# Kernel tuning notes

Measured on AMD Instinct MI355X. Metric: run time of the kernel, lower is better.

The kernel has to match this reference:

```python
import math
import jax, jax.numpy as jnp
import numpy as np

D_EMBD = 1024
N_HEAD = 16
BLOCK = 2048
B, T = 4, 2048


def setup_inputs() -> dict:
    key = jax.random.key(0)
    ks = jax.random.split(key, 5)
    d = D_EMBD
    return {
        "x": jax.random.normal(ks[0], (B, T, d), dtype=jnp.float32),
        "Wq": jax.random.normal(ks[1], (d, d), dtype=jnp.float32),
        "bq": jnp.zeros((d,), dtype=jnp.float32),
        "Wk": jax.random.normal(ks[2], (d, d), dtype=jnp.float32),
        "bk": jnp.zeros((d,), dtype=jnp.float32),
        "Wv": jax.random.normal(ks[3], (d, d), dtype=jnp.float32),
        "bv": jnp.zeros((d,), dtype=jnp.float32),
        "Wp": jax.random.normal(ks[4], (d, d), dtype=jnp.float32),
        "bp": jnp.zeros((d,), dtype=jnp.float32),
    }


def reference(x, Wq, bq, Wk, bk, Wv, bv, Wp, bp):
    Bb, Tt, C = x.shape
    n_head = N_HEAD
    hd = C // n_head  # head dim
    # QKV projections -> [B, H, T, hd]
    def split_heads(y):
        return y.reshape(Bb, Tt, n_head, hd).transpose(0, 2, 1, 3)
    Q = split_heads(x @ Wq + bq)
    K = split_heads(x @ Wk + bk)
    V = split_heads(x @ Wv + bv)
    # scores [B, H, T, T]
    attn = jnp.einsum('bhqd,bhkd->bhqk', Q, K) / math.sqrt(hd)
    # causal mask: -inf strictly above diagonal (matches triu(ones*-inf, 1))
    causal = jnp.tril(jnp.ones((Tt, Tt), dtype=bool))
    attn = jnp.where(causal, attn, -jnp.inf)
    attn = jax.nn.softmax(attn, axis=-1)
    y = jnp.einsum('bhqk,bhkd->bhqd', attn, V)
    y = y.transpose(0, 2, 1, 3).reshape(Bb, Tt, C)
    return y @ Wp + bp
```

## Files before the change

kernel.cpp:

```cpp
#include <hip/hip_runtime.h>
#include <stdint.h>
#include <stddef.h>

#define TT 2048
#define CC 1024
#define BBATCH 4
#define HH 16
#define HD 64
#define MTOT (BBATCH * TT)

typedef __bf16 bf16_t;
typedef __bf16 bf16x4 __attribute__((ext_vector_type(4)));
typedef __bf16 bf16x8 __attribute__((ext_vector_type(8)));
typedef float f32x4 __attribute__((ext_vector_type(4)));
typedef float f32x16 __attribute__((ext_vector_type(16)));

typedef const __attribute__((address_space(1))) uint32_t* as1_u32p;
typedef __attribute__((address_space(3))) uint32_t* as3_u32p;

__device__ __forceinline__ f32x4 mfma16(bf16x8 a, bf16x8 b, f32x4 c) {
  return __builtin_amdgcn_mfma_f32_16x16x32_bf16(a, b, c, 0, 0, 0);
}
__device__ __forceinline__ f32x16 mfma32(bf16x8 a, bf16x8 b, f32x16 c) {
  return __builtin_amdgcn_mfma_f32_32x32x16_bf16(a, b, c, 0, 0, 0);
}

__device__ __forceinline__ void gload_lds16(void* lds, const void* g) {
  __builtin_amdgcn_global_load_lds((as1_u32p)g, (as3_u32p)lds, 16, 0, 0);
}

__device__ __forceinline__ bf16x8 rd32(const char* t, int row, int lane) {
  int sl = (lane >> 4) ^ ((row >> 1) & 3);
  return *(const bf16x8*)(t + row * 64 + sl * 16);
}
__device__ __forceinline__ bf16x8 rd32r(const char* t, int row, int slot) {
  return *(const bf16x8*)(t + row * 128 + ((slot ^ (row & 7)) * 16));
}

__global__ void split_x_kernel(const float* __restrict__ x, bf16_t* __restrict__ xh,
                               bf16_t* __restrict__ xl, int n4) {
  int stride = gridDim.x * blockDim.x;
  for (int i = blockIdx.x * blockDim.x + threadIdx.x; i < n4; i += stride) {
    float4 v = ((const float4*)x)[i];
    float vv[4] = {v.x, v.y, v.z, v.w};
    bf16x4 hv, lv;
#pragma unroll
    for (int j = 0; j < 4; ++j) {
      bf16_t h = (bf16_t)vv[j];
      hv[j] = h;
      lv[j] = (bf16_t)(vv[j] - (float)h);
    }
    *(bf16x4*)(xh + (size_t)i * 4) = hv;
    *(bf16x4*)(xl + (size_t)i * 4) = lv;
  }
}

__global__ void transpose_split_kernel(const float* __restrict__ Wq, const float* __restrict__ Wk,
                                       const float* __restrict__ Wv, const float* __restrict__ Wp,
                                       bf16_t* __restrict__ wqkh, bf16_t* __restrict__ wqkl,
                                       bf16_t* __restrict__ wv_t, bf16_t* __restrict__ wp_t) {
  __shared__ float tile[32][33];
  int mat = blockIdx.z;
  const float* W = (mat == 0) ? Wq : (mat == 1) ? Wk : (mat == 2) ? Wv : Wp;
  int tx = threadIdx.x, ty = threadIdx.y;
  int n0 = blockIdx.x * 32, k0 = blockIdx.y * 32;
#pragma unroll
  for (int j = 0; j < 32; j += 8)
    tile[ty + j][tx] = W[(size_t)(k0 + ty + j) * CC + n0 + tx];
  __syncthreads();
#pragma unroll
  for (int j = 0; j < 32; j += 8) {
    float v = tile[tx][ty + j];
    int n = n0 + ty + j, k = k0 + tx;
    if (mat <= 1) {
      bf16_t h = (bf16_t)v;
      size_t o = (size_t)(mat * CC + n) * CC + k;
      wqkh[o] = h;
      wqkl[o] = (bf16_t)(v - (float)h);
    } else {
      bf16_t* dst = (mat == 2) ? wv_t : wp_t;
      dst[(size_t)n * CC + k] = (bf16_t)v;
    }
  }
}

__global__ __launch_bounds__(512, 2) void gemm_qk_kernel(
    const bf16_t* __restrict__ Ah, const bf16_t* __restrict__ Al,
    const bf16_t* __restrict__ Bh, const bf16_t* __restrict__ Bl,
    const float* __restrict__ bq, const float* __restrict__ bk,
    bf16_t* __restrict__ qh, bf16_t* __restrict__ ql,
    bf16_t* __restrict__ kh, bf16_t* __restrict__ kl) {
  __shared__ __align__(16) char s_ah[2][16384];
  __shared__ __align__(16) char s_al[2][16384];
  __shared__ __align__(16) char s_bh[2][16384];
  __shared__ __align__(16) char s_bl[2][16384];

  const int blk = blockIdx.x;
  const int bn = blk & 7;
  const int bm = blk >> 3;
  const int tid = threadIdx.x, w = tid >> 6, lane = tid & 63;
  const int wr = w >> 2, wc = w & 3;
  const int qi = lane & 15, hi = lane >> 4;

  const int c0 = w * 2, c1 = w * 2 + 1;
  const int srow0 = c0 * 16 + (lane >> 2);
  const int srow1 = c1 * 16 + (lane >> 2);
  const int ssl0 = (lane & 3) ^ ((srow0 >> 1) & 3);
  const int ssl1 = (lane & 3) ^ ((srow1 >> 1) & 3);
  const size_t a_off0 = (size_t)(bm * 256 + srow0) * CC + ssl0 * 8;
  const size_t a_off1 = (size_t)(bm * 256 + srow1) * CC + ssl1 * 8;
  const size_t b_off0 = (size_t)(bn * 256 + srow0) * CC + ssl0 * 8;
  const size_t b_off1 = (size_t)(bn * 256 + srow1) * CC + ssl1 * 8;

  f32x4 acc[8][4] = {};

#define STAGE_QK(buf, k0)                                        \
  do {                                                           \
    gload_lds16(s_ah[buf] + c0 * 1024, Ah + a_off0 + (k0));      \
    gload_lds16(s_ah[buf] + c1 * 1024, Ah + a_off1 + (k0));      \
    gload_lds16(s_al[buf] + c0 * 1024, Al + a_off0 + (k0));      \
    gload_lds16(s_al[buf] + c1 * 1024, Al + a_off1 + (k0));      \
    gload_lds16(s_bh[buf] + c0 * 1024, Bh + b_off0 + (k0));      \
    gload_lds16(s_bh[buf] + c1 * 1024, Bh + b_off1 + (k0));      \
    gload_lds16(s_bl[buf] + c0 * 1024, Bl + b_off0 + (k0));      \
    gload_lds16(s_bl[buf] + c1 * 1024, Bl + b_off1 + (k0));      \
  } while (0)

  STAGE_QK(0, 0);
  int cur = 0;
  for (int ks = 0; ks < 32; ++ks) {
    if (ks < 31) {
      STAGE_QK(cur ^ 1, (ks + 1) * 32);
      asm volatile("s_waitcnt vmcnt(8)" ::: "memory");
    } else {
      asm volatile("s_waitcnt vmcnt(0)" ::: "memory");
    }
    __builtin_amdgcn_s_barrier();

    bf16x8 bfh[4], bfl[4];
#pragma unroll
    for (int ni = 0; ni < 4; ++ni) {
      int br = wc * 64 + ni * 16 + qi;
      bfh[ni] = rd32(s_bh[cur], br, lane);
      bfl[ni] = rd32(s_bl[cur], br, lane);
    }
    __builtin_amdgcn_s_setprio(1);
#pragma unroll
    for (int mi = 0; mi < 8; ++mi) {
      int ar = wr * 128 + mi * 16 + qi;
      bf16x8 ahf = rd32(s_ah[cur], ar, lane);
      bf16x8 alf = rd32(s_al[cur], ar, lane);
#pragma unroll
      for (int ni = 0; ni < 4; ++ni) {
        acc[mi][ni] = mfma16(ahf, bfh[ni], acc[mi][ni]);
        acc[mi][ni] = mfma16(ahf, bfl[ni], acc[mi][ni]);
        acc[mi][ni] = mfma16(alf, bfh[ni], acc[mi][ni]);
      }
    }
    __builtin_amdgcn_s_setprio(0);
    asm volatile("s_waitcnt lgkmcnt(0)" ::: "memory");
    __builtin_amdgcn_s_barrier();
    cur ^= 1;
  }
#undef STAGE_QK

  const int which = bn >> 2;
  const float* bias = which ? bk : bq;
  bf16_t* oh = which ? kh : qh;
  bf16_t* ol = which ? kl : ql;
#pragma unroll
  for (int mi = 0; mi < 8; ++mi) {
#pragma unroll
    for (int ni = 0; ni < 4; ++ni) {
      const int col = bn * 256 + wc * 64 + ni * 16 + qi;
      const int c1i = col & 1023;
      const int h = c1i >> 6, d = c1i & 63;
#pragma unroll
      for (int r = 0; r < 4; ++r) {
        const int row = bm * 256 + wr * 128 + mi * 16 + hi * 4 + r;
        const int b = row >> 11, t = row & 2047;
        float v = acc[mi][ni][r] + bias[c1i];
        if (!which) v *= 0.125f;
        const size_t off = ((size_t)(b * HH + h) * TT + t) * HD + d;
        bf16_t hv = (bf16_t)v;
        oh[off] = hv;
        ol[off] = (bf16_t)(v - (float)hv);
      }
    }
  }
}

template <int MODE>
__global__ __launch_bounds__(256) void gemm_kernel(
    const bf16_t* __restrict__ Ah,
    const bf16_t* __restrict__ Bh,
    const float* __restrict__ bias0,
    void* __restrict__ out0) {
  __shared__ __align__(16) char smem[2 * 8192];
  char* sAh = smem;
  char* sBh = smem + 8192;

  const int bn = blockIdx.x, bm = blockIdx.y;
  const int tid = threadIdx.x, w = tid >> 6, lane = tid & 63;
  const int wr = w >> 1, wc = w & 1;

  f32x4 acc[4][4] = {};

  for (int ks = 0; ks < 32; ++ks) {
    const int k0 = ks * 32;
    __syncthreads();
#pragma unroll
    for (int it = 0; it < 2; ++it) {
      int c = it * 4 + w;
      int row = c * 16 + (lane >> 2);
      int sl = (lane & 3) ^ ((row >> 1) & 3);
      size_t aoff = (size_t)(bm * 128 + row) * CC + k0 + sl * 8;
      size_t boff = (size_t)(bn * 128 + row) * CC + k0 + sl * 8;
      gload_lds16(sAh + c * 1024, Ah + aoff);
      gload_lds16(sBh + c * 1024, Bh + boff);
    }
    __syncthreads();

    bf16x8 afh[4], bfh[4];
#pragma unroll
    for (int i = 0; i < 4; ++i) {
      int ar = wr * 64 + i * 16 + (lane & 15);
      int br = wc * 64 + i * 16 + (lane & 15);
      afh[i] = rd32(sAh, ar, lane);
      bfh[i] = rd32(sBh, br, lane);
    }
#pragma unroll
    for (int mi = 0; mi < 4; ++mi) {
#pragma unroll
      for (int ni = 0; ni < 4; ++ni) {
        acc[mi][ni] = mfma16(afh[mi], bfh[ni], acc[mi][ni]);
      }
    }
  }

#pragma unroll
  for (int mi = 0; mi < 4; ++mi) {
#pragma unroll
    for (int ni = 0; ni < 4; ++ni) {
      const int col = bn * 128 + wc * 64 + ni * 16 + (lane & 15);
#pragma unroll
      for (int r = 0; r < 4; ++r) {
        const int row = bm * 128 + wr * 64 + mi * 16 + (lane >> 4) * 4 + r;
        float v = acc[mi][ni][r];
        if (MODE == 1) {
          const int h = col >> 6, d = col & 63;
          const int b = row >> 11, t = row & 2047;
          float vv = v + bias0[col];
          ((bf16_t*)out0)[((size_t)(b * HH + h) * HD + d) * TT + t] = (bf16_t)vv;
        } else {
          ((float*)out0)[(size_t)row * CC + col] = v + bias0[col];
        }
      }
    }
  }
}

__global__ __launch_bounds__(256, 3) void attn_kernel(
    const bf16_t* __restrict__ qh, const bf16_t* __restrict__ ql,
    const bf16_t* __restrict__ kh, const bf16_t* __restrict__ kl,
    const bf16_t* __restrict__ vt, bf16_t* __restrict__ y) {
  __shared__ __align__(16) char s_kh[2][8192];
  __shared__ __align__(16) char s_kl[2][8192];
  __shared__ __align__(16) char s_vt[2][8192];

  const int blk = blockIdx.x;
  const int qb = 15 - (blk >> 6);
  const int bh = (blk & 7) * 8 + ((blk >> 3) & 7);
  const int b = bh >> 4, h = bh & 15;
  const int tid = threadIdx.x, w = tid >> 6, lane = tid & 63;
  const int l31 = lane & 31, hi = lane >> 5;

  const int strow0 = w * 16 + (lane >> 3);
  const int strow1 = strow0 + 8;
  const int sl0 = (lane & 7) ^ (strow0 & 7);
  const int sl1 = (lane & 7) ^ (strow1 & 7);
  const int ksrow0 = (strow0 & ~12) | ((strow0 & 4) << 1) | ((strow0 & 8) >> 1);
  const int ksrow1 = (strow1 & ~12) | ((strow1 & 4) << 1) | ((strow1 & 8) >> 1);
  const size_t koff0 = ((size_t)bh * TT + ksrow0) * HD + sl0 * 8;
  const size_t koff1 = ((size_t)bh * TT + ksrow1) * HD + sl1 * 8;
  const size_t voff0 = ((size_t)bh * HD + strow0) * TT + sl0 * 8;
  const size_t voff1 = ((size_t)bh * HD + strow1) * TT + sl1 * 8;
  const int ch0 = (w * 2) * 1024, ch1 = (w * 2 + 1) * 1024;

#define STAGE_ATTN(buf, kt)                                                  \
  do {                                                                       \
    gload_lds16(s_kh[buf] + ch0, kh + koff0 + (size_t)(kt) * 64 * HD);       \
    gload_lds16(s_kh[buf] + ch1, kh + koff1 + (size_t)(kt) * 64 * HD);       \
    gload_lds16(s_kl[buf] + ch0, kl + koff0 + (size_t)(kt) * 64 * HD);       \
    gload_lds16(s_kl[buf] + ch1, kl + koff1 + (size_t)(kt) * 64 * HD);       \
    gload_lds16(s_vt[buf] + ch0, vt + voff0 + (size_t)(kt) * 64);            \
    gload_lds16(s_vt[buf] + ch1, vt + voff1 + (size_t)(kt) * 64);            \
  } while (0)

  const int ktmax = 2 * qb + 1;
  const int qrow0 = qb * 128 + w * 32;
  const int qv = qrow0 + l31;

  bf16x8 qhf[4], qlf[4];
#pragma unroll
  for (int kc = 0; kc < 4; ++kc) {
    size_t off = ((size_t)bh * TT + qv) * HD + kc * 16 + hi * 8;
    qhf[kc] = *(const bf16x8*)(qh + off);
    qlf[kc] = *(const bf16x8*)(ql + off);
  }

  f32x16 o0 = {}, o1 = {};
  float m = -1e30f, l = 0.f;

  STAGE_ATTN(0, 0);
  int cur = 0;
  for (int kt = 0; kt <= ktmax; ++kt) {
    if (kt < ktmax) {
      STAGE_ATTN(cur ^ 1, kt + 1);
      asm volatile("s_waitcnt vmcnt(6)" ::: "memory");
    } else {
      asm volatile("s_waitcnt vmcnt(0)" ::: "memory");
    }
    __builtin_amdgcn_s_barrier();

    const char* ckh = s_kh[cur];
    const char* ckl = s_kl[cur];
    const char* cvt = s_vt[cur];
    const bool active = (qrow0 + 31 >= kt * 64);
    if (active) {
      f32x16 s0 = {}, s1 = {};
#pragma unroll
      for (int kc = 0; kc < 4; ++kc) {
        bf16x8 kfh = rd32r(ckh, l31, kc * 2 + hi);
        bf16x8 kfl = rd32r(ckl, l31, kc * 2 + hi);
        s0 = mfma32(kfh, qhf[kc], s0);
        s0 = mfma32(kfl, qhf[kc], s0);
        s0 = mfma32(kfh, qlf[kc], s0);
      }
#pragma unroll
      for (int kc = 0; kc < 4; ++kc) {
        bf16x8 kfh = rd32r(ckh, 32 + l31, kc * 2 + hi);
        bf16x8 kfl = rd32r(ckl, 32 + l31, kc * 2 + hi);
        s1 = mfma32(kfh, qhf[kc], s1);
        s1 = mfma32(kfl, qhf[kc], s1);
        s1 = mfma32(kfh, qlf[kc], s1);
      }

      if (kt * 64 + 63 > qrow0) {
#pragma unroll
        for (int r = 0; r < 16; ++r) {
          const int kvb = kt * 64 + (r & 7) + 8 * hi + 16 * (r >> 3);
          if (kvb > qv) s0[r] = -1e30f;
          if (kvb + 32 > qv) s1[r] = -1e30f;
        }
      }

      float t8[8];
#pragma unroll
      for (int r = 0; r < 8; ++r)
        t8[r] = fmaxf(fmaxf(s0[r], s0[r + 8]), fmaxf(s1[r], s1[r + 8]));
      float t4a = fmaxf(t8[0], t8[4]), t4b = fmaxf(t8[1], t8[5]);
      float t4c = fmaxf(t8[2], t8[6]), t4d = fmaxf(t8[3], t8[7]);
      float tmax = fmaxf(fmaxf(t4a, t4b), fmaxf(t4c, t4d));
      tmax = fmaxf(tmax, __shfl_xor(tmax, 32));

      const float mnew = fmaxf(m, tmax);
      if (!__all(tmax <= m)) {
        const float sc = __expf(m - mnew);
        l *= sc;
#pragma unroll
        for (int r = 0; r < 16; ++r) { o0[r] *= sc; o1[r] *= sc; }
        m = mnew;
      }

#pragma unroll
      for (int r = 0; r < 16; ++r) {
        s0[r] = __expf(s0[r] - m);
        s1[r] = __expf(s1[r] - m);
      }
      float p8[8];
#pragma unroll
      for (int r = 0; r < 8; ++r)
        p8[r] = (s0[r] + s0[r + 8]) + (s1[r] + s1[r + 8]);
      float ps = ((p8[0] + p8[1]) + (p8[2] + p8[3])) + ((p8[4] + p8[5]) + (p8[6] + p8[7]));
      ps += __shfl_xor(ps, 32);
      l += ps;

      bf16x8 pa[4];
#pragma unroll
      for (int cc = 0; cc < 4; ++cc) {
#pragma unroll
        for (int j = 0; j < 8; ++j)
          pa[cc][j] = (bf16_t)((cc >> 1) ? s1[8 * (cc & 1) + j] : s0[8 * (cc & 1) + j]);
      }

#pragma unroll
      for (int cc = 0; cc < 4; ++cc) {
        bf16x8 vf0 = rd32r(cvt, l31, cc * 2 + hi);
        bf16x8 vf1 = rd32r(cvt, 32 + l31, cc * 2 + hi);
        o0 = mfma32(vf0, pa[cc], o0);
        o1 = mfma32(vf1, pa[cc], o1);
      }
    }

    asm volatile("s_waitcnt lgkmcnt(0)" ::: "memory");
    __builtin_amdgcn_s_barrier();
    cur ^= 1;
  }

  const float inv = 1.f / l;
  bf16_t* yb = y + (size_t)(b * TT + qv) * CC + h * HD;
#pragma unroll
  for (int g = 0; g < 4; ++g) {
    bf16x4 ov0, ov1;
#pragma unroll
    for (int r = 0; r < 4; ++r) {
      ov0[r] = (bf16_t)(o0[g * 4 + r] * inv);
      ov1[r] = (bf16_t)(o1[g * 4 + r] * inv);
    }
    *(bf16x4*)(yb + g * 8 + hi * 4) = ov0;
    *(bf16x4*)(yb + 32 + g * 8 + hi * 4) = ov1;
  }
#undef STAGE_ATTN
}

extern "C" void kernel_launch(void* const* d_in, const int* in_sizes, int n_in,
                              void* d_out, int out_size, void* d_ws, size_t ws_size,
                              hipStream_t stream) {
  (void)in_sizes; (void)n_in; (void)out_size; (void)ws_size;
  const float* x  = (const float*)d_in[0];
  const float* Wq = (const float*)d_in[1];
  const float* bq = (const float*)d_in[2];
  const float* Wk = (const float*)d_in[3];
  const float* bk = (const float*)d_in[4];
  const float* Wv = (const float*)d_in[5];
  const float* bv = (const float*)d_in[6];
  const float* Wp = (const float*)d_in[7];
  const float* bp = (const float*)d_in[8];

  char* ws = (char*)d_ws;
  const size_t MB = 1024 * 1024;
  bf16_t* xh   = (bf16_t*)(ws + 0 * MB);
  bf16_t* xl   = (bf16_t*)(ws + 16 * MB);
  bf16_t* wqkh = (bf16_t*)(ws + 32 * MB);
  bf16_t* wqkl = (bf16_t*)(ws + 36 * MB);
  bf16_t* wv_t = (bf16_t*)(ws + 40 * MB);
  bf16_t* wp_t = (bf16_t*)(ws + 42 * MB);
  bf16_t* qhw  = (bf16_t*)(ws + 44 * MB);
  bf16_t* qlw  = (bf16_t*)(ws + 60 * MB);
  bf16_t* khw  = (bf16_t*)(ws + 76 * MB);
  bf16_t* klw  = (bf16_t*)(ws + 92 * MB);
  bf16_t* vtw  = (bf16_t*)(ws + 108 * MB);
  bf16_t* yw   = (bf16_t*)(ws + 124 * MB);

  split_x_kernel<<<2048, 256, 0, stream>>>(x, xh, xl, MTOT * CC / 4);
  transpose_split_kernel<<<dim3(32, 32, 4), dim3(32, 8), 0, stream>>>(
      Wq, Wk, Wv, Wp, wqkh, wqkl, wv_t, wp_t);
  gemm_qk_kernel<<<256, 512, 0, stream>>>(
      xh, xl, wqkh, wqkl, bq, bk, qhw, qlw, khw, klw);
  gemm_kernel<1><<<dim3(8, 64), 256, 0, stream>>>(
      xh, wv_t, bv, vtw);
  attn_kernel<<<1024, 256, 0, stream>>>(qhw, qlw, khw, klw, vtw, yw);
  gemm_kernel<2><<<dim3(8, 64), 256, 0, stream>>>(
      yw, wp_t, bp, d_out);
}
```

Before: 247.0 us.

## Rewrite V and output-projection GEMMs with 256x128 tiles and double-buffered LDS

Replaces the 128x128 single-buffered GEMM used for the V projection and the output projection with a 512-thread kernel on 256x128 tiles. The next k-slice is prefetched into a second LDS buffer while the current one feeds the MFMAs, gated by explicit vmcnt waits and raw barriers, and s_setprio is raised around the MFMA block. The grid drops from 512 to 256 blocks, so fewer waves are available to hide latency, and LDS use per block doubles.

```diff
diff --git a/kernel.cpp b/kernel.cpp
--- a/kernel.cpp
+++ b/kernel.cpp
@@ -191,69 +191,82 @@
 }
 
 template <int MODE>
-__global__ __launch_bounds__(256) void gemm_kernel(
-    const bf16_t* __restrict__ Ah,
-    const bf16_t* __restrict__ Bh,
-    const float* __restrict__ bias0,
-    void* __restrict__ out0) {
-  __shared__ __align__(16) char smem[2 * 8192];
-  char* sAh = smem;
-  char* sBh = smem + 8192;
-
-  const int bn = blockIdx.x, bm = blockIdx.y;
+__global__ __launch_bounds__(512, 2) void gemm2_kernel(
+    const bf16_t* __restrict__ A, const bf16_t* __restrict__ B,
+    const float* __restrict__ bias, void* __restrict__ out) {
+  __shared__ __align__(16) char s_a[2][16384];
+  __shared__ __align__(16) char s_b[2][8192];
+
+  const int blk = blockIdx.x;
+  const int bn = blk & 7;
+  const int bm = blk >> 3;
   const int tid = threadIdx.x, w = tid >> 6, lane = tid & 63;
-  const int wr = w >> 1, wc = w & 1;
-
-  f32x4 acc[4][4] = {};
-
+  const int wr = w >> 2, wc = w & 3;
+  const int qi = lane & 15, hi = lane >> 4;
+
+  const int arow0 = (w * 2) * 16 + (lane >> 2);
+  const int arow1 = (w * 2 + 1) * 16 + (lane >> 2);
+  const int brow = w * 16 + (lane >> 2);
+  const int asl0 = (lane & 3) ^ ((arow0 >> 1) & 3);
+  const int asl1 = (lane & 3) ^ ((arow1 >> 1) & 3);
+  const int bsl = (lane & 3) ^ ((brow >> 1) & 3);
+  const size_t a_off0 = (size_t)(bm * 256 + arow0) * CC + asl0 * 8;
+  const size_t a_off1 = (size_t)(bm * 256 + arow1) * CC + asl1 * 8;
+  const size_t b_off = (size_t)(bn * 128 + brow) * CC + bsl * 8;
+
+  f32x4 acc[8][2] = {};
+
+#define STAGE2(buf, k0)                                               \
+  do {                                                                \
+    gload_lds16(s_a[buf] + (w * 2) * 1024, A + a_off0 + (k0));        \
+    gload_lds16(s_a[buf] + (w * 2 + 1) * 1024, A + a_off1 + (k0));    \
+    gload_lds16(s_b[buf] + w * 1024, B + b_off + (k0));               \
+  } while (0)
+
+  STAGE2(0, 0);
+  int cur = 0;
   for (int ks = 0; ks < 32; ++ks) {
-    const int k0 = ks * 32;
-    __syncthreads();
-#pragma unroll
-    for (int it = 0; it < 2; ++it) {
-      int c = it * 4 + w;
-      int row = c * 16 + (lane >> 2);
-      int sl = (lane & 3) ^ ((row >> 1) & 3);
-      size_t aoff = (size_t)(bm * 128 + row) * CC + k0 + sl * 8;
-      size_t boff = (size_t)(bn * 128 + row) * CC + k0 + sl * 8;
-      gload_lds16(sAh + c * 1024, Ah + aoff);
-      gload_lds16(sBh + c * 1024, Bh + boff);
-    }
-    __syncthreads();
-
-    bf16x8 afh[4], bfh[4];
-#pragma unroll
-    for (int i = 0; i < 4; ++i) {
-      int ar = wr * 64 + i * 16 + (lane & 15);
-      int br = wc * 64 + i * 16 + (lane & 15);
-      afh[i] = rd32(sAh, ar, lane);
-      bfh[i] = rd32(sBh, br, lane);
-    }
-#pragma unroll
-    for (int mi = 0; mi < 4; ++mi) {
-#pragma unroll
-      for (int ni = 0; ni < 4; ++ni) {
-        acc[mi][ni] = mfma16(afh[mi], bfh[ni], acc[mi][ni]);
-      }
-    }
-  }
-
-#pragma unroll
-  for (int mi = 0; mi < 4; ++mi) {
-#pragma unroll
-    for (int ni = 0; ni < 4; ++ni) {
-      const int col = bn * 128 + wc * 64 + ni * 16 + (lane & 15);
+    if (ks < 31) {
+      STAGE2(cur ^ 1, (ks + 1) * 32);
+      asm volatile("s_waitcnt vmcnt(3)" ::: "memory");
+    } else {
+      asm volatile("s_waitcnt vmcnt(0)" ::: "memory");
+    }
+    __builtin_amdgcn_s_barrier();
+
+    bf16x8 bf[2];
+#pragma unroll
+    for (int ni = 0; ni < 2; ++ni)
+      bf[ni] = rd32(s_b[cur], wc * 32 + ni * 16 + qi, lane);
+    __builtin_amdgcn_s_setprio(1);
+#pragma unroll
+    for (int mi = 0; mi < 8; ++mi) {
+      bf16x8 af = rd32(s_a[cur], wr * 128 + mi * 16 + qi, lane);
+      acc[mi][0] = mfma16(af, bf[0], acc[mi][0]);
+      acc[mi][1] = mfma16(af, bf[1], acc[mi][1]);
+    }
+    __builtin_amdgcn_s_setprio(0);
+    asm volatile("s_waitcnt lgkmcnt(0)" ::: "memory");
+    __builtin_amdgcn_s_barrier();
+    cur ^= 1;
+  }
+#undef STAGE2
+
+#pragma unroll
+  for (int mi = 0; mi < 8; ++mi) {
+#pragma unroll
+    for (int ni = 0; ni < 2; ++ni) {
+      const int col = bn * 128 + wc * 32 + ni * 16 + qi;
 #pragma unroll
       for (int r = 0; r < 4; ++r) {
-        const int row = bm * 128 + wr * 64 + mi * 16 + (lane >> 4) * 4 + r;
-        float v = acc[mi][ni][r];
+        const int row = bm * 256 + wr * 128 + mi * 16 + hi * 4 + r;
+        const float v = acc[mi][ni][r] + bias[col];
         if (MODE == 1) {
           const int h = col >> 6, d = col & 63;
           const int b = row >> 11, t = row & 2047;
-          float vv = v + bias0[col];
-          ((bf16_t*)out0)[((size_t)(b * HH + h) * HD + d) * TT + t] = (bf16_t)vv;
+          ((bf16_t*)out)[((size_t)(b * HH + h) * HD + d) * TT + t] = (bf16_t)v;
         } else {
-          ((float*)out0)[(size_t)row * CC + col] = v + bias0[col];
+          ((float*)out)[(size_t)row * CC + col] = v;
         }
       }
     }
@@ -458,9 +471,7 @@
       Wq, Wk, Wv, Wp, wqkh, wqkl, wv_t, wp_t);
   gemm_qk_kernel<<<256, 512, 0, stream>>>(
       xh, xl, wqkh, wqkl, bq, bk, qhw, qlw, khw, klw);
-  gemm_kernel<1><<<dim3(8, 64), 256, 0, stream>>>(
-      xh, wv_t, bv, vtw);
+  gemm2_kernel<1><<<256, 512, 0, stream>>>(xh, wv_t, bv, vtw);
   attn_kernel<<<1024, 256, 0, stream>>>(qhw, qlw, khw, klw, vtw, yw);
-  gemm_kernel<2><<<dim3(8, 64), 256, 0, stream>>>(
-      yw, wp_t, bp, d_out);
-}
+  gemm2_kernel<2><<<256, 512, 0, stream>>>(yw, wp_t, bp, d_out);
+}
```

Result: slower. 265.6 us (+7.5%).
